# Performance work log

Hardware: AMD Instinct MI355X
Metric: run time of the kernel (lower is better)

## Reference

```python
import jax, jax.numpy as jnp
import numpy as np

RADIUS = 0.25
NUM_NEIGHBORS = 32
POS_DIM = 24
STEM_C = 64
PATCH_C = 256
LN_EPS = 1e-5


def query_ball_point(radius, nsample, xyz, new_xyz):
    # xyz: [B,N,3], new_xyz: [B,S,3] -> idx [B,S,nsample] (PointNet++ ball query)
    N = xyz.shape[1]
    sqr = (jnp.sum(new_xyz ** 2, -1)[:, :, None]
           + jnp.sum(xyz ** 2, -1)[:, None, :]
           - 2.0 * jnp.einsum('bsd,bnd->bsn', new_xyz, xyz))  # [B,S,N]
    idx = jnp.broadcast_to(jnp.arange(N, dtype=jnp.int32), sqr.shape)
    idx = jnp.where(sqr > radius * radius, N, idx)
    idx = jnp.sort(idx, axis=-1)[..., :nsample]  # first nsample in-ball (by index order)
    first = idx[..., :1]
    idx = jnp.where(idx == N, first, idx)  # pad empty slots with first neighbor
    return idx


def index_points(points, idx):
    # points [B,N,C], idx [B,S,K] -> [B,S,K,C]
    return jax.vmap(lambda p, i: p[i])(points, idx)


def rel_pos_encoding(rel_xyz, dim=POS_DIM):
    # sinusoidal Fourier encoding of 3D offsets: 3 coords * 2 (sin,cos) * dim//6 freqs
    nf = dim // 6
    freqs = 2.0 ** jnp.arange(nf, dtype=rel_xyz.dtype)
    ang = rel_xyz[..., None] * freqs  # [...,3,nf]
    enc = jnp.concatenate([jnp.sin(ang), jnp.cos(ang)], axis=-1)  # [...,3,2nf]
    return enc.reshape(rel_xyz.shape[:-1] + (dim,))


def point_mlp(x, W, b, gamma, beta, activate):
    h = jnp.einsum('...i,io->...o', x, W) + b
    mu = jnp.mean(h, -1, keepdims=True)
    var = jnp.mean((h - mu) ** 2, -1, keepdims=True)
    h = (h - mu) * jax.lax.rsqrt(var + LN_EPS) * gamma + beta
    return jax.nn.gelu(h, approximate=False) if activate else h


def setup_inputs() -> dict:
    key = jax.random.key(0)
    ks = jax.random.split(key, 8)
    B, N, S = 8, 16384, 1024
    in_c = STEM_C + 3 + POS_DIM  # 91
    return {
        'xyz': jax.random.uniform(ks[0], (B, N, 3), dtype=jnp.float32),
        'point_feature': jax.random.normal(ks[1], (B, N, STEM_C), dtype=jnp.float32),
        'patch_center': jax.random.uniform(ks[2], (B, S, 3), dtype=jnp.float32),
        'W1': jax.random.normal(ks[3], (in_c, PATCH_C), dtype=jnp.float32) * 0.02,
        'b1': jnp.zeros((PATCH_C,), jnp.float32),
        'g1': jnp.ones((PATCH_C,), jnp.float32),
        'be1': jnp.zeros((PATCH_C,), jnp.float32),
        'W2': jax.random.normal(ks[4], (PATCH_C, PATCH_C), dtype=jnp.float32) * 0.02,
        'b2': jnp.zeros((PATCH_C,), jnp.float32),
        'g2': jnp.ones((PATCH_C,), jnp.float32),
        'be2': jnp.zeros((PATCH_C,), jnp.float32),
    }


def reference(xyz, point_feature, patch_center, W1, b1, g1, be1, W2, b2, g2, be2):
    neighbor_idx = query_ball_point(RADIUS, NUM_NEIGHBORS, xyz, patch_center)  # [B,S,K]
    grouped_xyz = index_points(xyz, neighbor_idx)              # [B,S,K,3]
    grouped_feature = index_points(point_feature, neighbor_idx)  # [B,S,K,C]
    relative_xyz = grouped_xyz - patch_center[:, :, None, :]
    relative_position = rel_pos_encoding(relative_xyz)         # [B,S,K,24]
    grouped_input = jnp.concatenate((grouped_feature, relative_xyz, relative_position), axis=-1)
    h = point_mlp(grouped_input, W1, b1, g1, be1, True)
    h = point_mlp(h, W2, b2, g2, be2, False)
    patch_feature = jnp.max(h, axis=2)                         # max over neighbors -> [B,S,PATCH_C]
    return patch_feature, neighbor_idx
```

## Files before the change

kernel.cpp:

```cpp
#include <hip/hip_runtime.h>
#include <math.h>

#define NPTS 16384
#define KN 32
#define C 256
#define NQ 8192
#define PF_ELEMS (NQ * C)

#define W1P_ELEMS (3 * 16 * 64 * 8)
#define W2P_ELEMS (8 * 16 * 64 * 8)
#define HSTR 264

typedef _Float16 half8 __attribute__((ext_vector_type(8)));
typedef _Float16 half4v __attribute__((ext_vector_type(4)));
typedef _Float16 half2t __attribute__((ext_vector_type(2)));
typedef float f32x4 __attribute__((ext_vector_type(4)));

union H8u { half8 v; half2t h2[4]; };

__device__ __forceinline__ float fdot2f(half2t a, half2t b, float c) {
#if __has_builtin(__builtin_amdgcn_fdot2)
    return __builtin_amdgcn_fdot2(a, b, c, false);
#else
    return fmaf((float)a[1], (float)b[1], fmaf((float)a[0], (float)b[0], c));
#endif
}

__device__ __forceinline__ float gelu_tanh(float x) {
    const float t  = x * x;
    const float p2 = fmaf(t, 0.0713548162726f, 1.59576912161f);
    const float e  = __expf(x * p2);
    return x - x * __builtin_amdgcn_rcpf(e + 1.0f);
}

__device__ __forceinline__ void stat8(const H8u& u, half2t ones, float& s, float& s2) {
    #pragma unroll
    for (int j = 0; j < 4; ++j) {
        s  = fdot2f(u.h2[j], ones, s);
        s2 = fdot2f(u.h2[j], u.h2[j], s2);
    }
}

__device__ __forceinline__ void norm_gelu8(H8u& u, const H8u& g, const H8u& be,
                                           half2t rsh, half2t nmuh) {
    #pragma unroll
    for (int j = 0; j < 4; ++j) {
        const half2t A = g.h2[j] * rsh;
        const half2t B = A * nmuh + be.h2[j];
        const half2t y = u.h2[j] * A + B;
        half2t o;
        o[0] = (_Float16)gelu_tanh((float)y[0]);
        o[1] = (_Float16)gelu_tanh((float)y[1]);
        u.h2[j] = o;
    }
}

__device__ __forceinline__ void norm8(H8u& u, const H8u& g, const H8u& be,
                                      half2t rsh, half2t nmuh) {
    #pragma unroll
    for (int j = 0; j < 4; ++j) {
        const half2t A = g.h2[j] * rsh;
        const half2t B = A * nmuh + be.h2[j];
        u.h2[j] = u.h2[j] * A + B;
    }
}

__global__ void prep_w_kernel(const float* __restrict__ W1,
                              const float* __restrict__ W2,
                              _Float16* __restrict__ wp) {
    const int idx = blockIdx.x * 256 + threadIdx.x;
    if (idx < 96 * 256) {
        const int k = idx >> 8, n = idx & 255;
        const float v = (k < 91) ? W1[k * 256 + n] : 0.0f;
        const int kt = k >> 5, quad = (k >> 3) & 3, j = k & 7;
        const int nt = n >> 4, l15 = n & 15;
        wp[(((kt * 16 + nt) * 64) + quad * 16 + l15) * 8 + j] = (_Float16)v;
    } else {
        const int e = idx - 96 * 256;
        const int k = e >> 8, n = e & 255;
        const int kt = k >> 5, quad = (k >> 3) & 3, j = k & 7;
        const int nt = n >> 4, l15 = n & 15;
        wp[W1P_ELEMS + (((kt * 16 + nt) * 64) + quad * 16 + l15) * 8 + j] =
            (_Float16)W2[k * 256 + n];
    }
}

__global__ void __launch_bounds__(256, 6)
encoder_fused(const float* __restrict__ xyz,
              const float* __restrict__ pf,
              const float* __restrict__ ctr,
              const float* __restrict__ b1, const float* __restrict__ g1,
              const float* __restrict__ be1,
              const float* __restrict__ b2, const float* __restrict__ g2,
              const float* __restrict__ be2,
              const _Float16* __restrict__ w1p,
              const _Float16* __restrict__ w2p,
              float* __restrict__ out0,
              float* __restrict__ out1) {
    const int q = blockIdx.x;
    const int b = q >> 10;
    const int t = threadIdx.x;
    const int w = t >> 6;
    const int lane = t & 63;
    const int quad = lane >> 4;
    const int l15  = lane & 15;

    __shared__ __align__(16) unsigned char H16raw[KN * HSTR * 2];
    __shared__ __align__(16) unsigned char Xsraw[KN * 104 * 2];
    __shared__ __align__(16) _Float16 lnph[4 * 256];
    __shared__ int nbr[KN];
    __shared__ int wcnt[2][4];

    _Float16 (*H16)[HSTR] = (_Float16(*)[HSTR])H16raw;
    _Float16 (*Xs)[104]   = (_Float16(*)[104])Xsraw;
    _Float16* g1h  = lnph;
    _Float16* be1h = lnph + 256;
    _Float16* g2h  = lnph + 512;
    _Float16* be2h = lnph + 768;

    lnph[t]       = (_Float16)g1[t];
    lnph[256 + t] = (_Float16)be1[t];
    lnph[512 + t] = (_Float16)g2[t];
    lnph[768 + t] = (_Float16)be2[t];

    const float* xb = xyz + (size_t)b * NPTS * 3;
    const float cx = ctr[q * 3 + 0];
    const float cy = ctr[q * 3 + 1];
    const float cz = ctr[q * 3 + 2];
    const float sc = __fadd_rn(__fadd_rn(__fmul_rn(cx, cx), __fmul_rn(cy, cy)),
                               __fmul_rn(cz, cz));

    int found = 0;
    int par = 0;
    for (int base = 0; base < NPTS; base += 256) {
        const int n = base + t;
        const float px = xb[n * 3 + 0];
        const float py = xb[n * 3 + 1];
        const float pz = xb[n * 3 + 2];
        const float sp = __fadd_rn(__fadd_rn(__fmul_rn(px, px), __fmul_rn(py, py)),
                                   __fmul_rn(pz, pz));
        const float dt = __fadd_rn(__fadd_rn(__fmul_rn(cx, px), __fmul_rn(cy, py)),
                                   __fmul_rn(cz, pz));
        const float sqr = __fsub_rn(__fadd_rn(sc, sp), __fmul_rn(2.0f, dt));
        const bool inball = (sqr <= 0.0625f);

        const unsigned long long m = __ballot(inball);
        if (lane == 0) wcnt[par][w] = (int)__popcll(m);
        __syncthreads();
        int pre = found;
        if (w > 0) pre += wcnt[par][0];
        if (w > 1) pre += wcnt[par][1];
        if (w > 2) pre += wcnt[par][2];
        const int tot = found + wcnt[par][0] + wcnt[par][1] + wcnt[par][2] + wcnt[par][3];
        const int pos = pre + (int)__popcll(m & ((1ull << lane) - 1ull));
        if (inball && pos < KN) nbr[pos] = n;
        found = tot;
        par ^= 1;
        if (found >= KN) break;
    }
    __syncthreads();
    const int count = (found < KN) ? found : KN;
    const int first = (count > 0) ? nbr[0] : NPTS;

    if (t < KN)
        out1[(size_t)q * KN + t] = (float)((t < count) ? nbr[t] : first);

    {
        const int k  = t >> 3;
        const int tc = t & 7;
        const int nidx = (k < count) ? nbr[k] : first;
        const int n = (nidx < NPTS) ? nidx : NPTS - 1;
        const float rx = xb[n * 3 + 0] - cx;
        const float ry = xb[n * 3 + 1] - cy;
        const float rz = xb[n * 3 + 2] - cz;
        const float* pfr = pf + ((size_t)b * NPTS + n) * 64;

        const float4 f0 = *(const float4*)(pfr + tc * 8);
        const float4 f1 = *(const float4*)(pfr + tc * 8 + 4);
        half8 hv;
        hv[0] = (_Float16)f0.x; hv[1] = (_Float16)f0.y;
        hv[2] = (_Float16)f0.z; hv[3] = (_Float16)f0.w;
        hv[4] = (_Float16)f1.x; hv[5] = (_Float16)f1.y;
        hv[6] = (_Float16)f1.z; hv[7] = (_Float16)f1.w;
        *(half8*)&Xs[k][tc * 8] = hv;

        half4v ov;
        #pragma unroll
        for (int j = 0; j < 4; ++j) {
            const int c = 64 + tc * 4 + j;
            float v;
            if (c < 67) {
                v = (c == 64) ? rx : ((c == 65) ? ry : rz);
            } else if (c < 91) {
                const int jj = c - 67;
                const int d = jj >> 3;
                const int mm = jj & 7;
                const float f = (float)(1 << (mm & 3));
                const float r = (d == 0) ? rx : ((d == 1) ? ry : rz);
                v = (mm < 4) ? __sinf(r * f) : __cosf(r * f);
            } else {
                v = 0.0f;
            }
            ov[j] = (_Float16)v;
        }
        *(half4v*)&Xs[k][64 + tc * 4] = ov;
    }
    __syncthreads();

    const int qx = (quad ^ (l15 >> 2)) * 8;

    f32x4 acc[2][4];

    #pragma unroll
    for (int mt = 0; mt < 2; ++mt)
        #pragma unroll
        for (int nt = 0; nt < 4; ++nt)
            acc[mt][nt] = (f32x4){0.f, 0.f, 0.f, 0.f};

    #pragma unroll
    for (int kt = 0; kt < 3; ++kt) {
        const half8 a0 = *(const half8*)&Xs[l15][kt * 32 + quad * 8];
        const half8 a1 = *(const half8*)&Xs[16 + l15][kt * 32 + quad * 8];
        #pragma unroll
        for (int nt = 0; nt < 4; ++nt) {
            const int ntg = w * 4 + nt;
            const half8 bf = *(const half8*)&w1p[((kt * 16 + ntg) * 64 + lane) * 8];
            acc[0][nt] = __builtin_amdgcn_mfma_f32_16x16x32_f16(a0, bf, acc[0][nt], 0, 0, 0);
            acc[1][nt] = __builtin_amdgcn_mfma_f32_16x16x32_f16(a1, bf, acc[1][nt], 0, 0, 0);
        }
    }
    #pragma unroll
    for (int nt = 0; nt < 4; ++nt) {
        const int col  = w * 64 + nt * 16 + l15;
        const int colp = col ^ (quad << 3);
        const float bb = b1[col];
        #pragma unroll
        for (int mt = 0; mt < 2; ++mt)
            #pragma unroll
            for (int r = 0; r < 4; ++r)
                H16[16 * mt + 4 * quad + r][colp] = (_Float16)(acc[mt][nt][r] + bb);
    }
    __syncthreads();

    const int row  = t >> 3;
    const int p    = t & 7;
    const int qrow = (row >> 2) & 3;
    _Float16* hb = &H16[row][0];
    const int a0o = (( 2 * p    ) ^ qrow) << 3;
    const int a1o = (( 2 * p + 1) ^ qrow) << 3;
    const int a2o = ((16 + 2 * p) ^ qrow) << 3;
    const int a3o = ((17 + 2 * p) ^ qrow) << 3;
    half2t ones;
    ones[0] = (_Float16)1.0f;
    ones[1] = (_Float16)1.0f;

    {
        H8u u0, u1, u2, u3;
        u0.v = *(const half8*)(hb + a0o);
        u1.v = *(const half8*)(hb + a1o);
        u2.v = *(const half8*)(hb + a2o);
        u3.v = *(const half8*)(hb + a3o);

        float s = 0.0f, s2 = 0.0f;
        stat8(u0, ones, s, s2); stat8(u1, ones, s, s2);
        stat8(u2, ones, s, s2); stat8(u3, ones, s, s2);
        #pragma unroll
        for (int off = 1; off < 8; off <<= 1) {
            s  += __shfl_xor(s, off, 64);
            s2 += __shfl_xor(s2, off, 64);
        }
        const float mu  = s * (1.0f / 256.0f);
        const float var = fmaf(s2, 1.0f / 256.0f, -mu * mu);
        const float rs  = __builtin_amdgcn_rsqf(var + 1e-5f);
        half2t rsh, nmuh;
        rsh[0]  = (_Float16)rs;    rsh[1]  = (_Float16)rs;
        nmuh[0] = (_Float16)(-mu); nmuh[1] = (_Float16)(-mu);

        H8u gA0, gA1, gB0, gB1, bA0, bA1, bB0, bB1;
        gA0.v = *(const half8*)&g1h[16 * p];        bA0.v = *(const half8*)&be1h[16 * p];
        gA1.v = *(const half8*)&g1h[16 * p + 8];    bA1.v = *(const half8*)&be1h[16 * p + 8];
        gB0.v = *(const half8*)&g1h[128 + 16 * p];  bB0.v = *(const half8*)&be1h[128 + 16 * p];
        gB1.v = *(const half8*)&g1h[136 + 16 * p];  bB1.v = *(const half8*)&be1h[136 + 16 * p];

        norm_gelu8(u0, gA0, bA0, rsh, nmuh);
        norm_gelu8(u1, gA1, bA1, rsh, nmuh);
        norm_gelu8(u2, gB0, bB0, rsh, nmuh);
        norm_gelu8(u3, gB1, bB1, rsh, nmuh);

        *(half8*)(hb + a0o) = u0.v;
        *(half8*)(hb + a1o) = u1.v;
        *(half8*)(hb + a2o) = u2.v;
        *(half8*)(hb + a3o) = u3.v;
    }
    __syncthreads();

    #pragma unroll
    for (int mt = 0; mt < 2; ++mt)
        #pragma unroll
        for (int nt = 0; nt < 4; ++nt)
            acc[mt][nt] = (f32x4){0.f, 0.f, 0.f, 0.f};

    #pragma unroll
    for (int kt = 0; kt < 8; ++kt) {
        const half8 a0 = *(const half8*)&H16[l15][kt * 32 + qx];
        const half8 a1 = *(const half8*)&H16[16 + l15][kt * 32 + qx];
        #pragma unroll
        for (int nt = 0; nt < 4; ++nt) {
            const int ntg = w * 4 + nt;
            const half8 bf = *(const half8*)&w2p[((kt * 16 + ntg) * 64 + lane) * 8];
            acc[0][nt] = __builtin_amdgcn_mfma_f32_16x16x32_f16(a0, bf, acc[0][nt], 0, 0, 0);
            acc[1][nt] = __builtin_amdgcn_mfma_f32_16x16x32_f16(a1, bf, acc[1][nt], 0, 0, 0);
        }
    }
    __syncthreads();
    #pragma unroll
    for (int nt = 0; nt < 4; ++nt) {
        const int col  = w * 64 + nt * 16 + l15;
        const int colp = col ^ (quad << 3);
        const float bb = b2[col];
        #pragma unroll
        for (int mt = 0; mt < 2; ++mt)
            #pragma unroll
            for (int r = 0; r < 4; ++r)
                H16[16 * mt + 4 * quad + r][colp] = (_Float16)(acc[mt][nt][r] + bb);
    }
    __syncthreads();

    {
        H8u u0, u1, u2, u3;
        u0.v = *(const half8*)(hb + a0o);
        u1.v = *(const half8*)(hb + a1o);
        u2.v = *(const half8*)(hb + a2o);
        u3.v = *(const half8*)(hb + a3o);

        float s = 0.0f, s2 = 0.0f;
        stat8(u0, ones, s, s2); stat8(u1, ones, s, s2);
        stat8(u2, ones, s, s2); stat8(u3, ones, s, s2);
        #pragma unroll
        for (int off = 1; off < 8; off <<= 1) {
            s  += __shfl_xor(s, off, 64);
            s2 += __shfl_xor(s2, off, 64);
        }
        const float mu  = s * (1.0f / 256.0f);
        const float var = fmaf(s2, 1.0f / 256.0f, -mu * mu);
        const float rs  = __builtin_amdgcn_rsqf(var + 1e-5f);
        half2t rsh, nmuh;
        rsh[0]  = (_Float16)rs;    rsh[1]  = (_Float16)rs;
        nmuh[0] = (_Float16)(-mu); nmuh[1] = (_Float16)(-mu);

        H8u gA0, gA1, gB0, gB1, bA0, bA1, bB0, bB1;
        gA0.v = *(const half8*)&g2h[16 * p];        bA0.v = *(const half8*)&be2h[16 * p];
        gA1.v = *(const half8*)&g2h[16 * p + 8];    bA1.v = *(const half8*)&be2h[16 * p + 8];
        gB0.v = *(const half8*)&g2h[128 + 16 * p];  bB0.v = *(const half8*)&be2h[128 + 16 * p];
        gB1.v = *(const half8*)&g2h[136 + 16 * p];  bB1.v = *(const half8*)&be2h[136 + 16 * p];

        norm8(u0, gA0, bA0, rsh, nmuh);
        norm8(u1, gA1, bA1, rsh, nmuh);
        norm8(u2, gB0, bB0, rsh, nmuh);
        norm8(u3, gB1, bB1, rsh, nmuh);

        *(half8*)(hb + a0o) = u0.v;
        *(half8*)(hb + a1o) = u1.v;
        *(half8*)(hb + a2o) = u2.v;
        *(half8*)(hb + a3o) = u3.v;
    }
    __syncthreads();

    if (t < 128) {
        const _Float16* Hf = &H16[0][0];
        const int c = t >> 2;
        const int o = (2 * t) & 7;
        half2t mx = *(const half2t*)(Hf + (c << 3) + o);
        #pragma unroll
        for (int r = 1; r < KN; ++r) {
            const half2t v = *(const half2t*)(Hf + r * HSTR + ((c ^ ((r >> 2) & 3)) << 3) + o);
            mx = __builtin_elementwise_max(mx, v);
        }
        float2 o2;
        o2.x = (float)mx[0];
        o2.y = (float)mx[1];
        *(float2*)&out0[(size_t)q * C + 2 * t] = o2;
    }
}

extern "C" void kernel_launch(void* const* d_in, const int* in_sizes, int n_in,
                              void* d_out, int out_size, void* d_ws, size_t ws_size,
                              hipStream_t stream) {
    const float* xyz = (const float*)d_in[0];
    const float* pf  = (const float*)d_in[1];
    const float* ctr = (const float*)d_in[2];
    const float* W1  = (const float*)d_in[3];
    const float* b1  = (const float*)d_in[4];
    const float* g1  = (const float*)d_in[5];
    const float* be1 = (const float*)d_in[6];
    const float* W2  = (const float*)d_in[7];
    const float* b2  = (const float*)d_in[8];
    const float* g2  = (const float*)d_in[9];
    const float* be2 = (const float*)d_in[10];

    float* out = (float*)d_out;
    _Float16* wp = (_Float16*)d_ws;

    prep_w_kernel<<<(96 * 256 + 65536) / 256, 256, 0, stream>>>(W1, W2, wp);
    encoder_fused<<<NQ, 256, 0, stream>>>(xyz, pf, ctr,
                                          b1, g1, be1, b2, g2, be2,
                                          wp, wp + W1P_ELEMS,
                                          out, out + PF_ELEMS);
}
```

Measured before the change: 191.2 us.

## Fold bias into W1, alias Xs onto H16, transpose MFMA outputs for vector stores

Folds b1 into W1 as an extra input row, with a constant-1 input column at index 91, so the first layer's bias add disappears. Aliases the Xs staging buffer onto H16 shared memory to cut LDS use and raises launch bounds to 7 blocks per SM. Swaps the MFMA operands so each lane holds 4 consecutive channels, which allows half4 vector stores into an unswizzled H16 layout and simpler LN and max-reduction indexing. An extra barrier guards the aliased buffer, and removing the XOR swizzle may bring back LDS bank conflicts.

```diff
diff --git a/kernel.cpp b/kernel.cpp
--- a/kernel.cpp
+++ b/kernel.cpp
@@ -66,12 +66,13 @@
 }
 
 __global__ void prep_w_kernel(const float* __restrict__ W1,
+                              const float* __restrict__ b1,
                               const float* __restrict__ W2,
                               _Float16* __restrict__ wp) {
     const int idx = blockIdx.x * 256 + threadIdx.x;
     if (idx < 96 * 256) {
         const int k = idx >> 8, n = idx & 255;
-        const float v = (k < 91) ? W1[k * 256 + n] : 0.0f;
+        const float v = (k < 91) ? W1[k * 256 + n] : ((k == 91) ? b1[n] : 0.0f);
         const int kt = k >> 5, quad = (k >> 3) & 3, j = k & 7;
         const int nt = n >> 4, l15 = n & 15;
         wp[(((kt * 16 + nt) * 64) + quad * 16 + l15) * 8 + j] = (_Float16)v;
@@ -85,12 +86,11 @@
     }
 }
 
-__global__ void __launch_bounds__(256, 6)
+__global__ void __launch_bounds__(256, 7)
 encoder_fused(const float* __restrict__ xyz,
               const float* __restrict__ pf,
               const float* __restrict__ ctr,
-              const float* __restrict__ b1, const float* __restrict__ g1,
-              const float* __restrict__ be1,
+              const float* __restrict__ g1, const float* __restrict__ be1,
               const float* __restrict__ b2, const float* __restrict__ g2,
               const float* __restrict__ be2,
               const _Float16* __restrict__ w1p,
@@ -106,13 +106,12 @@
     const int l15  = lane & 15;
 
     __shared__ __align__(16) unsigned char H16raw[KN * HSTR * 2];
-    __shared__ __align__(16) unsigned char Xsraw[KN * 104 * 2];
     __shared__ __align__(16) _Float16 lnph[4 * 256];
     __shared__ int nbr[KN];
     __shared__ int wcnt[2][4];
 
     _Float16 (*H16)[HSTR] = (_Float16(*)[HSTR])H16raw;
-    _Float16 (*Xs)[104]   = (_Float16(*)[104])Xsraw;
+    _Float16 (*Xs)[104]   = (_Float16(*)[104])H16raw;
     _Float16* g1h  = lnph;
     _Float16* be1h = lnph + 256;
     _Float16* g2h  = lnph + 512;
@@ -198,6 +197,8 @@
                 const float f = (float)(1 << (mm & 3));
                 const float r = (d == 0) ? rx : ((d == 1) ? ry : rz);
                 v = (mm < 4) ? __sinf(r * f) : __cosf(r * f);
+            } else if (c == 91) {
+                v = 1.0f;
             } else {
                 v = 0.0f;
             }
@@ -207,8 +208,6 @@
     }
     __syncthreads();
 
-    const int qx = (quad ^ (l15 >> 2)) * 8;
-
     f32x4 acc[2][4];
 
     #pragma unroll
@@ -219,47 +218,45 @@
 
     #pragma unroll
     for (int kt = 0; kt < 3; ++kt) {
-        const half8 a0 = *(const half8*)&Xs[l15][kt * 32 + quad * 8];
-        const half8 a1 = *(const half8*)&Xs[16 + l15][kt * 32 + quad * 8];
+        const half8 x0 = *(const half8*)&Xs[l15][kt * 32 + quad * 8];
+        const half8 x1 = *(const half8*)&Xs[16 + l15][kt * 32 + quad * 8];
         #pragma unroll
         for (int nt = 0; nt < 4; ++nt) {
-            const int ntg = w * 4 + nt;
-            const half8 bf = *(const half8*)&w1p[((kt * 16 + ntg) * 64 + lane) * 8];
-            acc[0][nt] = __builtin_amdgcn_mfma_f32_16x16x32_f16(a0, bf, acc[0][nt], 0, 0, 0);
-            acc[1][nt] = __builtin_amdgcn_mfma_f32_16x16x32_f16(a1, bf, acc[1][nt], 0, 0, 0);
-        }
-    }
+            const half8 wf = *(const half8*)&w1p[((kt * 16 + w * 4 + nt) * 64 + lane) * 8];
+            acc[0][nt] = __builtin_amdgcn_mfma_f32_16x16x32_f16(wf, x0, acc[0][nt], 0, 0, 0);
+            acc[1][nt] = __builtin_amdgcn_mfma_f32_16x16x32_f16(wf, x1, acc[1][nt], 0, 0, 0);
+        }
+    }
+    __syncthreads();
+
     #pragma unroll
     for (int nt = 0; nt < 4; ++nt) {
-        const int col  = w * 64 + nt * 16 + l15;
-        const int colp = col ^ (quad << 3);
-        const float bb = b1[col];
-        #pragma unroll
-        for (int mt = 0; mt < 2; ++mt)
+        const int chb = (w * 4 + nt) * 16 + quad * 4;
+        #pragma unroll
+        for (int mt = 0; mt < 2; ++mt) {
+            half4v h;
             #pragma unroll
             for (int r = 0; r < 4; ++r)
-                H16[16 * mt + 4 * quad + r][colp] = (_Float16)(acc[mt][nt][r] + bb);
-    }
-    __syncthreads();
-
-    const int row  = t >> 3;
-    const int p    = t & 7;
-    const int qrow = (row >> 2) & 3;
-    _Float16* hb = &H16[row][0];
-    const int a0o = (( 2 * p    ) ^ qrow) << 3;
-    const int a1o = (( 2 * p + 1) ^ qrow) << 3;
-    const int a2o = ((16 + 2 * p) ^ qrow) << 3;
-    const int a3o = ((17 + 2 * p) ^ qrow) << 3;
+                h[r] = (_Float16)acc[mt][nt][r];
+            *(half4v*)&H16[mt * 16 + l15][chb] = h;
+        }
+    }
+    __syncthreads();
+
+    const int row = t >> 3;
+    const int p   = t & 7;
+    _Float16* hrow0 = &H16[row][16 * p];
+    _Float16* hrow1 = &H16[row][128 + 16 * p];
     half2t ones;
     ones[0] = (_Float16)1.0f;
     ones[1] = (_Float16)1.0f;
 
     {
         H8u u0, u1, u2, u3;
-        u0.v = *(const half8*)(hb + a0o);
-        u1.v = *(const half8*)(hb + a1o);
-        u2.v = *(const half8*)(hb + a2o);
-        u3.v = *(const half8*)(hb + a3o);
+        u0.v = *(const half8*)hrow0;
+        u1.v = *(const half8*)(hrow0 + 8);
+        u2.v = *(const half8*)hrow1;
+        u3.v = *(const half8*)(hrow1 + 8);
 
         float s = 0.0f, s2 = 0.0f;
         stat8(u0, ones, s, s2); stat8(u1, ones, s, s2);
@@ -287,10 +284,10 @@
         norm_gelu8(u2, gB0, bB0, rsh, nmuh);
         norm_gelu8(u3, gB1, bB1, rsh, nmuh);
 
-        *(half8*)(hb + a0o) = u0.v;
-        *(half8*)(hb + a1o) = u1.v;
-        *(half8*)(hb + a2o) = u2.v;
-        *(half8*)(hb + a3o) = u3.v;
+        *(half8*)hrow0       = u0.v;
+        *(half8*)(hrow0 + 8) = u1.v;
+        *(half8*)hrow1       = u2.v;
+        *(half8*)(hrow1 + 8) = u3.v;
     }
     __syncthreads();
 
@@ -302,36 +299,38 @@
 
     #pragma unroll
     for (int kt = 0; kt < 8; ++kt) {
-        const half8 a0 = *(const half8*)&H16[l15][kt * 32 + qx];
-        const half8 a1 = *(const half8*)&H16[16 + l15][kt * 32 + qx];
+        const half8 h0 = *(const half8*)&H16[l15][kt * 32 + quad * 8];
+        const half8 h1 = *(const half8*)&H16[16 + l15][kt * 32 + quad * 8];
         #pragma unroll
         for (int nt = 0; nt < 4; ++nt) {
-            const int ntg = w * 4 + nt;
-            const half8 bf = *(const half8*)&w2p[((kt * 16 + ntg) * 64 + lane) * 8];
-            acc[0][nt] = __builtin_amdgcn_mfma_f32_16x16x32_f16(a0, bf, acc[0][nt], 0, 0, 0);
-            acc[1][nt] = __builtin_amdgcn_mfma_f32_16x16x32_f16(a1, bf, acc[1][nt], 0, 0, 0);
-        }
-    }
-    __syncthreads();
+            const half8 wf = *(const half8*)&w2p[((kt * 16 + w * 4 + nt) * 64 + lane) * 8];
+            acc[0][nt] = __builtin_amdgcn_mfma_f32_16x16x32_f16(wf, h0, acc[0][nt], 0, 0, 0);
+            acc[1][nt] = __builtin_amdgcn_mfma_f32_16x16x32_f16(wf, h1, acc[1][nt], 0, 0, 0);
+        }
+    }
+    __syncthreads();
+
     #pragma unroll
     for (int nt = 0; nt < 4; ++nt) {
-        const int col  = w * 64 + nt * 16 + l15;
-        const int colp = col ^ (quad << 3);
-        const float bb = b2[col];
-        #pragma unroll
-        for (int mt = 0; mt < 2; ++mt)
+        const int chb = (w * 4 + nt) * 16 + quad * 4;
+        const f32x4 bv = *(const f32x4*)&b2[chb];
+        #pragma unroll
+        for (int mt = 0; mt < 2; ++mt) {
+            half4v h;
             #pragma unroll
             for (int r = 0; r < 4; ++r)
-                H16[16 * mt + 4 * quad + r][colp] = (_Float16)(acc[mt][nt][r] + bb);
+                h[r] = (_Float16)(acc[mt][nt][r] + bv[r]);
+            *(half4v*)&H16[mt * 16 + l15][chb] = h;
+        }
     }
     __syncthreads();
 
     {
         H8u u0, u1, u2, u3;
-        u0.v = *(const half8*)(hb + a0o);
-        u1.v = *(const half8*)(hb + a1o);
-        u2.v = *(const half8*)(hb + a2o);
-        u3.v = *(const half8*)(hb + a3o);
+        u0.v = *(const half8*)hrow0;
+        u1.v = *(const half8*)(hrow0 + 8);
+        u2.v = *(const half8*)hrow1;
+        u3.v = *(const half8*)(hrow1 + 8);
 
         float s = 0.0f, s2 = 0.0f;
         stat8(u0, ones, s, s2); stat8(u1, ones, s, s2);
@@ -359,21 +358,19 @@
         norm8(u2, gB0, bB0, rsh, nmuh);
         norm8(u3, gB1, bB1, rsh, nmuh);
 
-        *(half8*)(hb + a0o) = u0.v;
-        *(half8*)(hb + a1o) = u1.v;
-        *(half8*)(hb + a2o) = u2.v;
-        *(half8*)(hb + a3o) = u3.v;
+        *(half8*)hrow0       = u0.v;
+        *(half8*)(hrow0 + 8) = u1.v;
+        *(half8*)hrow1       = u2.v;
+        *(half8*)(hrow1 + 8) = u3.v;
     }
     __syncthreads();
 
     if (t < 128) {
         const _Float16* Hf = &H16[0][0];
-        const int c = t >> 2;
-        const int o = (2 * t) & 7;
-        half2t mx = *(const half2t*)(Hf + (c << 3) + o);
+        half2t mx = *(const half2t*)(Hf + 2 * t);
         #pragma unroll
         for (int r = 1; r < KN; ++r) {
-            const half2t v = *(const half2t*)(Hf + r * HSTR + ((c ^ ((r >> 2) & 3)) << 3) + o);
+            const half2t v = *(const half2t*)(Hf + r * HSTR + 2 * t);
             mx = __builtin_elementwise_max(mx, v);
         }
         float2 o2;
@@ -401,9 +398,9 @@
     float* out = (float*)d_out;
     _Float16* wp = (_Float16*)d_ws;
 
-    prep_w_kernel<<<(96 * 256 + 65536) / 256, 256, 0, stream>>>(W1, W2, wp);
+    prep_w_kernel<<<(96 * 256 + 65536) / 256, 256, 0, stream>>>(W1, b1, W2, wp);
     encoder_fused<<<NQ, 256, 0, stream>>>(xyz, pf, ctr,
-                                          b1, g1, be1, b2, g2, be2,
+                                          g1, be1, b2, g2, be2,
                                           wp, wp + W1P_ELEMS,
                                           out, out + PF_ELEMS);
 }
```

Measured after the change: 192.7 us. About the same (+0.8%).
